# Kernel tuning notes

Measured on AMD Instinct MI355X. Metric: run time of the kernel, lower is better.

The kernel has to match this reference:

```python
import jax, jax.numpy as jnp
import numpy as np

N = 50000
E = 800000
F_IN = 128
HID = 64
HEADS = 4
NUM_TYPES = 1
NEG_SLOPE = 0.2


def setup_inputs() -> dict:
    key = jax.random.key(0)
    ks = jax.random.split(key, 20)
    s = 0.05
    inp = {
        "node_features": jax.random.normal(ks[0], (N, F_IN), jnp.float32),
        "node_types": jax.random.randint(ks[1], (N,), 0, NUM_TYPES, jnp.int32),
        "edge_index": jax.random.randint(ks[2], (2, E), 0, N, jnp.int32),
        # params
        "type_emb": jax.random.normal(ks[3], (NUM_TYPES, HID), jnp.float32) * s,
        "proj_w": jax.random.normal(ks[4], (F_IN, HID), jnp.float32) * s,
        "proj_b": jnp.zeros((HID,), jnp.float32),
        # GAT layer 0: in=64 -> heads*64, concat=True
        "lin_w0": jax.random.normal(ks[5], (HID, HEADS * HID), jnp.float32) * s,
        "att_src0": jax.random.normal(ks[6], (HEADS, HID), jnp.float32) * s,
        "att_dst0": jax.random.normal(ks[7], (HEADS, HID), jnp.float32) * s,
        "bias0": jnp.zeros((HEADS * HID,), jnp.float32),
        "ln_g0": jnp.ones((HEADS * HID,), jnp.float32),
        "ln_b0": jnp.zeros((HEADS * HID,), jnp.float32),
        # GAT layer 1: in=256 -> heads*64, concat=False (mean over heads)
        "lin_w1": jax.random.normal(ks[8], (HEADS * HID, HEADS * HID), jnp.float32) * s,
        "att_src1": jax.random.normal(ks[9], (HEADS, HID), jnp.float32) * s,
        "att_dst1": jax.random.normal(ks[10], (HEADS, HID), jnp.float32) * s,
        "bias1": jnp.zeros((HID,), jnp.float32),
        "ln_g1": jnp.ones((HID,), jnp.float32),
        "ln_b1": jnp.zeros((HID,), jnp.float32),
    }
    return inp


def _layer_norm(x, g, b, eps=1e-5):
    mu = jnp.mean(x, axis=-1, keepdims=True)
    var = jnp.mean(jnp.square(x - mu), axis=-1, keepdims=True)
    return (x - mu) * jax.lax.rsqrt(var + eps) * g + b


def _gat_conv(x, src, dst, lin_w, att_src, att_dst, bias, concat):
    # PyG GATConv: linear -> per-edge additive attention -> segment softmax over
    # incoming edges -> weighted scatter-sum. Self-loops already in src/dst.
    n = x.shape[0]
    H, C = att_src.shape
    h = (x @ lin_w).reshape(n, H, C)            # [N,H,C]
    a_s = jnp.sum(h * att_src[None], axis=-1)   # [N,H]
    a_d = jnp.sum(h * att_dst[None], axis=-1)   # [N,H]
    a = jax.nn.leaky_relu(a_s[src] + a_d[dst], NEG_SLOPE)  # [E,H]
    m = jax.ops.segment_max(a, dst, num_segments=n)
    e = jnp.exp(a - m[dst])
    z = jax.ops.segment_sum(e, dst, num_segments=n)
    alpha = e / z[dst]                           # [E,H]
    msg = h[src] * alpha[..., None]              # [E,H,C]
    out = jax.ops.segment_sum(msg, dst, num_segments=n)  # [N,H,C]
    if concat:
        out = out.reshape(n, H * C)
    else:
        out = out.mean(axis=1)
    return out + bias


def reference(node_features, node_types, edge_index,
              type_emb, proj_w, proj_b,
              lin_w0, att_src0, att_dst0, bias0, ln_g0, ln_b0,
              lin_w1, att_src1, att_dst1, bias1, ln_g1, ln_b1):
    n = node_features.shape[0]
    # add self loops (PyG GATConv default add_self_loops=True)
    loop = jnp.arange(n, dtype=edge_index.dtype)
    src = jnp.concatenate([edge_index[0], loop])
    dst = jnp.concatenate([edge_index[1], loop])

    x = node_features @ proj_w + proj_b + type_emb[node_types]  # [N,64]

    # layer 0: no residual (i == 0)
    x = _gat_conv(x, src, dst, lin_w0, att_src0, att_dst0, bias0, concat=True)
    x = jax.nn.relu(_layer_norm(x, ln_g0, ln_b0))  # [N,256]; dropout = identity (eval)

    # layer 1: residual shape [N,256] != output [N,64] -> residual skipped
    x = _gat_conv(x, src, dst, lin_w1, att_src1, att_dst1, bias1, concat=False)
    x = jax.nn.relu(_layer_norm(x, ln_g1, ln_b1))  # [N,64]
    return x
```

## Files before the change

### kernel.cpp

```cpp
#include <hip/hip_runtime.h>


#define BLK 256

typedef __bf16 bf16x8 __attribute__((ext_vector_type(8)));
typedef __bf16 bf16x4 __attribute__((ext_vector_type(4)));
typedef float  f32x4  __attribute__((ext_vector_type(4)));


__global__ __launch_bounds__(BLK) void k_deg(
    const int* __restrict__ dst, int* __restrict__ deg, int E, int n) {
  const int etot = E + n;
  for (int e = blockIdx.x * BLK + threadIdx.x; e < etot; e += gridDim.x * BLK) {
    int d = (e < E) ? dst[e] : (e - E);
    atomicAdd(&deg[d], 1);
  }
}

__global__ __launch_bounds__(BLK) void k_scan_chunk(
    const int* __restrict__ in, int* __restrict__ out, int* __restrict__ csum, int n) {
  const int b = blockIdx.x, t = threadIdx.x, i = b * BLK + t;
  const int lane = t & 63, w = t >> 6;
  int v = (i < n) ? in[i] : 0;
  int inc = v;
#pragma unroll
  for (int o = 1; o < 64; o <<= 1) {
    int tmp = __shfl_up(inc, o);
    if (lane >= o) inc += tmp;
  }
  __shared__ int ws[4];
  if (lane == 63) ws[w] = inc;
  __syncthreads();
  int off = 0;
  for (int k = 0; k < w; ++k) off += ws[k];
  if (i < n) out[i] = off + inc - v;
  if (t == BLK - 1 && csum) csum[b] = off + inc;
}

__global__ __launch_bounds__(BLK) void k_scan_add(
    int* __restrict__ rowstart, const int* __restrict__ chunkoff,
    int* __restrict__ cursor, int n) {
  for (int i = blockIdx.x * BLK + threadIdx.x; i < n; i += gridDim.x * BLK) {
    int r = rowstart[i] + chunkoff[i >> 8];
    rowstart[i] = r;
    cursor[i] = r;
  }
}

__global__ __launch_bounds__(BLK) void k_fill(
    const int* __restrict__ src, const int* __restrict__ dst,
    int* __restrict__ cursor, int* __restrict__ sidx, int E, int n) {
  const int etot = E + n;
  for (int e = blockIdx.x * BLK + threadIdx.x; e < etot; e += gridDim.x * BLK) {
    int s, d;
    if (e < E) { s = src[e]; d = dst[e]; } else { s = e - E; d = s; }
    int slot = atomicAdd(&cursor[d], 1);
    sidx[slot] = s;
  }
}


__global__ __launch_bounds__(BLK) void k_pack_w(
    const float* __restrict__ w, __bf16* __restrict__ wp, int K, int NC) {
  const int tot = (K >> 3) * NC;
  int idx = blockIdx.x * BLK + threadIdx.x;
  if (idx >= tot) return;
  int g = idx / NC, c = idx - g * NC;
#pragma unroll
  for (int j = 0; j < 8; ++j)
    wp[(size_t)idx * 8 + j] = (__bf16)w[(g * 8 + j) * NC + c];
}


__global__ __launch_bounds__(BLK) void k_proj_mfma(
    const float* __restrict__ nf, const int* __restrict__ types,
    const __bf16* __restrict__ pwp, const float* __restrict__ pb,
    const float* __restrict__ emb, __bf16* __restrict__ x0, int n) {
  const int t = threadIdx.x, w = t >> 6, l = t & 63;
  const int l15 = l & 15, lg = l >> 4;
  const int mbase = blockIdx.x * 64 + w * 16;
  f32x4 acc[4] = {};
  const int ar = mbase + l15;
  const bool av = ar < n;
#pragma unroll
  for (int ks = 0; ks < 4; ++ks) {
    bf16x8 a = {};
    if (av) {
      const float* ap = nf + (size_t)ar * 128 + ks * 32 + lg * 8;
      float4 f0 = *(const float4*)(ap);
      float4 f1 = *(const float4*)(ap + 4);
      a[0] = (__bf16)f0.x; a[1] = (__bf16)f0.y; a[2] = (__bf16)f0.z; a[3] = (__bf16)f0.w;
      a[4] = (__bf16)f1.x; a[5] = (__bf16)f1.y; a[6] = (__bf16)f1.z; a[7] = (__bf16)f1.w;
    }
#pragma unroll
    for (int nt = 0; nt < 4; ++nt) {
      int c = nt * 16 + l15;
      int g = ks * 4 + lg;
      bf16x8 b = *(const bf16x8*)(pwp + ((size_t)g * 64 + c) * 8);
      acc[nt] = __builtin_amdgcn_mfma_f32_16x16x32_bf16(a, b, acc[nt], 0, 0, 0);
    }
  }
#pragma unroll
  for (int reg = 0; reg < 4; ++reg) {
    int row = mbase + lg * 4 + reg;
    if (row < n) {
      int ty = types[row];
#pragma unroll
      for (int nt = 0; nt < 4; ++nt) {
        int c = nt * 16 + l15;
        x0[(size_t)row * 64 + c] = (__bf16)(acc[nt][reg] + pb[c] + emb[ty * 64 + c]);
      }
    }
  }
}


template <int K>
__global__ __launch_bounds__(BLK) void k_lin_mfma(
    const __bf16* __restrict__ X, const __bf16* __restrict__ Wp,
    const float* __restrict__ att_s, const float* __restrict__ att_d,
    __bf16* __restrict__ H, float* __restrict__ as_, float* __restrict__ ad_, int n) {
  const int t = threadIdx.x, w = t >> 6, l = t & 63;
  const int l15 = l & 15, lg = l >> 4;
  const int m0 = blockIdx.x * 64;

  float asv[4], adv[4];
#pragma unroll
  for (int nt = 0; nt < 4; ++nt) {
    int c = w * 64 + nt * 16 + l15;
    asv[nt] = att_s[c];
    adv[nt] = att_d[c];
  }

  f32x4 acc[4][4] = {};
  int rr[4];
  bool vv[4];
#pragma unroll
  for (int mt = 0; mt < 4; ++mt) { rr[mt] = m0 + mt * 16 + l15; vv[mt] = rr[mt] < n; }
  const bf16x8 zf = {};

  for (int ks = 0; ks < K / 32; ++ks) {
    bf16x8 a[4];
#pragma unroll
    for (int mt = 0; mt < 4; ++mt)
      a[mt] = vv[mt] ? *(const bf16x8*)(X + (size_t)rr[mt] * K + ks * 32 + lg * 8) : zf;
    bf16x8 b[4];
#pragma unroll
    for (int nt = 0; nt < 4; ++nt) {
      int c = w * 64 + nt * 16 + l15;
      int g = ks * 4 + lg;
      b[nt] = *(const bf16x8*)(Wp + ((size_t)g * 256 + c) * 8);
    }
#pragma unroll
    for (int nt = 0; nt < 4; ++nt)
#pragma unroll
      for (int mt = 0; mt < 4; ++mt)
        acc[mt][nt] = __builtin_amdgcn_mfma_f32_16x16x32_bf16(a[mt], b[nt], acc[mt][nt], 0, 0, 0);
  }

#pragma unroll
  for (int mt = 0; mt < 4; ++mt) {
#pragma unroll
    for (int reg = 0; reg < 4; ++reg) {
      int row = m0 + mt * 16 + lg * 4 + reg;
      bool vr = row < n;
      float s = 0.f, d = 0.f;
      if (vr) {
#pragma unroll
        for (int nt = 0; nt < 4; ++nt) {
          float cv = acc[mt][nt][reg];
          H[(size_t)row * 256 + w * 64 + nt * 16 + l15] = (__bf16)cv;
          s = fmaf(cv, asv[nt], s);
          d = fmaf(cv, adv[nt], d);
        }
      }
#pragma unroll
      for (int o = 8; o; o >>= 1) { s += __shfl_xor(s, o); d += __shfl_xor(d, o); }
      if (l15 == 0 && vr) { as_[row * 4 + w] = s; ad_[row * 4 + w] = d; }
    }
  }
}


__global__ __launch_bounds__(BLK) void k_agg0(
    const int* __restrict__ rowstart, const int* __restrict__ deg,
    const int* __restrict__ sidx, const float* __restrict__ as_,
    const float* __restrict__ ad_, const __bf16* __restrict__ h0,
    const float* __restrict__ bias, const float* __restrict__ g,
    const float* __restrict__ b, __bf16* __restrict__ x1, int n) {
  const int lane = threadIdx.x & 63;
  const int wid = (blockIdx.x * BLK + threadIdx.x) >> 6;
  const int nw = (gridDim.x * BLK) >> 6;
  const int hsel = lane >> 4;
  const float4 bias4 = ((const float4*)bias)[lane];
  const float4 g4 = ((const float4*)g)[lane];
  const float4 b4 = ((const float4*)b)[lane];
  for (int d = wid; d < n; d += nw) {
    const int start = rowstart[d], cnt = deg[d];
    const int* sp = sidx + start;
    const float adv = ad_[d * 4 + hsel];
    float ax = 0.f, ay = 0.f, az = 0.f, aw = 0.f, z = 0.f;
    int j = 0;
    for (; j + 4 <= cnt; j += 4) {
      int4 s4 = *(const int4*)(sp + j);
      int s0 = __builtin_amdgcn_readfirstlane(s4.x);
      int s1 = __builtin_amdgcn_readfirstlane(s4.y);
      int s2 = __builtin_amdgcn_readfirstlane(s4.z);
      int s3 = __builtin_amdgcn_readfirstlane(s4.w);
      float q0 = as_[s0 * 4 + hsel], q1 = as_[s1 * 4 + hsel];
      float q2 = as_[s2 * 4 + hsel], q3 = as_[s3 * 4 + hsel];
      bf16x4 v0 = *(const bf16x4*)(h0 + (size_t)s0 * 256 + lane * 4);
      bf16x4 v1 = *(const bf16x4*)(h0 + (size_t)s1 * 256 + lane * 4);
      bf16x4 v2 = *(const bf16x4*)(h0 + (size_t)s2 * 256 + lane * 4);
      bf16x4 v3 = *(const bf16x4*)(h0 + (size_t)s3 * 256 + lane * 4);
      float a;
      a = q0 + adv; a = fmaxf(a, 0.2f * a); float e0 = __expf(a);
      a = q1 + adv; a = fmaxf(a, 0.2f * a); float e1 = __expf(a);
      a = q2 + adv; a = fmaxf(a, 0.2f * a); float e2 = __expf(a);
      a = q3 + adv; a = fmaxf(a, 0.2f * a); float e3 = __expf(a);
      z += (e0 + e1) + (e2 + e3);
      ax = fmaf(e0, (float)v0[0], ax); ay = fmaf(e0, (float)v0[1], ay);
      az = fmaf(e0, (float)v0[2], az); aw = fmaf(e0, (float)v0[3], aw);
      ax = fmaf(e1, (float)v1[0], ax); ay = fmaf(e1, (float)v1[1], ay);
      az = fmaf(e1, (float)v1[2], az); aw = fmaf(e1, (float)v1[3], aw);
      ax = fmaf(e2, (float)v2[0], ax); ay = fmaf(e2, (float)v2[1], ay);
      az = fmaf(e2, (float)v2[2], az); aw = fmaf(e2, (float)v2[3], aw);
      ax = fmaf(e3, (float)v3[0], ax); ay = fmaf(e3, (float)v3[1], ay);
      az = fmaf(e3, (float)v3[2], az); aw = fmaf(e3, (float)v3[3], aw);
    }
    for (; j < cnt; ++j) {
      int s = __builtin_amdgcn_readfirstlane(sp[j]);
      float a = as_[s * 4 + hsel] + adv; a = fmaxf(a, 0.2f * a);
      float e = __expf(a);
      z += e;
      bf16x4 hv = *(const bf16x4*)(h0 + (size_t)s * 256 + lane * 4);
      ax = fmaf(e, (float)hv[0], ax); ay = fmaf(e, (float)hv[1], ay);
      az = fmaf(e, (float)hv[2], az); aw = fmaf(e, (float)hv[3], aw);
    }
    float rz = 1.f / z;
    float vx = ax * rz + bias4.x, vy = ay * rz + bias4.y;
    float vz = az * rz + bias4.z, vw = aw * rz + bias4.w;
    float s1 = vx + vy + vz + vw;
#pragma unroll
    for (int o = 32; o; o >>= 1) s1 += __shfl_xor(s1, o);
    float mu = s1 * (1.f / 256.f);
    float dx = vx - mu, dy = vy - mu, dz = vz - mu, dw = vw - mu;
    float q = dx * dx + dy * dy + dz * dz + dw * dw;
#pragma unroll
    for (int o = 32; o; o >>= 1) q += __shfl_xor(q, o);
    float is = rsqrtf(q * (1.f / 256.f) + 1e-5f);
    bf16x4 o4;
    o4[0] = (__bf16)fmaxf(dx * is * g4.x + b4.x, 0.f);
    o4[1] = (__bf16)fmaxf(dy * is * g4.y + b4.y, 0.f);
    o4[2] = (__bf16)fmaxf(dz * is * g4.z + b4.z, 0.f);
    o4[3] = (__bf16)fmaxf(dw * is * g4.w + b4.w, 0.f);
    *(bf16x4*)(x1 + (size_t)d * 256 + lane * 4) = o4;
  }
}

__global__ __launch_bounds__(BLK) void k_agg1(
    const int* __restrict__ rowstart, const int* __restrict__ deg,
    const int* __restrict__ sidx, const float* __restrict__ as_,
    const float* __restrict__ ad_, const __bf16* __restrict__ h1,
    const float* __restrict__ bias, const float* __restrict__ g,
    const float* __restrict__ b, float* __restrict__ out, int n) {
  const int lane = threadIdx.x & 63;
  const int wid = (blockIdx.x * BLK + threadIdx.x) >> 6;
  const int nw = (gridDim.x * BLK) >> 6;
  const int hsel = lane >> 4;
  const int p = lane & 15;
  const float4 bias4 = ((const float4*)bias)[p];
  const float4 g4 = ((const float4*)g)[p];
  const float4 b4 = ((const float4*)b)[p];
  for (int d = wid; d < n; d += nw) {
    const int start = rowstart[d], cnt = deg[d];
    const int* sp = sidx + start;
    const float adv = ad_[d * 4 + hsel];
    float ax = 0.f, ay = 0.f, az = 0.f, aw = 0.f, z = 0.f;
    int j = 0;
    for (; j + 4 <= cnt; j += 4) {
      int4 s4 = *(const int4*)(sp + j);
      int s0 = __builtin_amdgcn_readfirstlane(s4.x);
      int s1 = __builtin_amdgcn_readfirstlane(s4.y);
      int s2 = __builtin_amdgcn_readfirstlane(s4.z);
      int s3 = __builtin_amdgcn_readfirstlane(s4.w);
      float q0 = as_[s0 * 4 + hsel], q1 = as_[s1 * 4 + hsel];
      float q2 = as_[s2 * 4 + hsel], q3 = as_[s3 * 4 + hsel];
      bf16x4 v0 = *(const bf16x4*)(h1 + (size_t)s0 * 256 + lane * 4);
      bf16x4 v1 = *(const bf16x4*)(h1 + (size_t)s1 * 256 + lane * 4);
      bf16x4 v2 = *(const bf16x4*)(h1 + (size_t)s2 * 256 + lane * 4);
      bf16x4 v3 = *(const bf16x4*)(h1 + (size_t)s3 * 256 + lane * 4);
      float a;
      a = q0 + adv; a = fmaxf(a, 0.2f * a); float e0 = __expf(a);
      a = q1 + adv; a = fmaxf(a, 0.2f * a); float e1 = __expf(a);
      a = q2 + adv; a = fmaxf(a, 0.2f * a); float e2 = __expf(a);
      a = q3 + adv; a = fmaxf(a, 0.2f * a); float e3 = __expf(a);
      z += (e0 + e1) + (e2 + e3);
      ax = fmaf(e0, (float)v0[0], ax); ay = fmaf(e0, (float)v0[1], ay);
      az = fmaf(e0, (float)v0[2], az); aw = fmaf(e0, (float)v0[3], aw);
      ax = fmaf(e1, (float)v1[0], ax); ay = fmaf(e1, (float)v1[1], ay);
      az = fmaf(e1, (float)v1[2], az); aw = fmaf(e1, (float)v1[3], aw);
      ax = fmaf(e2, (float)v2[0], ax); ay = fmaf(e2, (float)v2[1], ay);
      az = fmaf(e2, (float)v2[2], az); aw = fmaf(e2, (float)v2[3], aw);
      ax = fmaf(e3, (float)v3[0], ax); ay = fmaf(e3, (float)v3[1], ay);
      az = fmaf(e3, (float)v3[2], az); aw = fmaf(e3, (float)v3[3], aw);
    }
    for (; j < cnt; ++j) {
      int s = __builtin_amdgcn_readfirstlane(sp[j]);
      float a = as_[s * 4 + hsel] + adv; a = fmaxf(a, 0.2f * a);
      float e = __expf(a);
      z += e;
      bf16x4 hv = *(const bf16x4*)(h1 + (size_t)s * 256 + lane * 4);
      ax = fmaf(e, (float)hv[0], ax); ay = fmaf(e, (float)hv[1], ay);
      az = fmaf(e, (float)hv[2], az); aw = fmaf(e, (float)hv[3], aw);
    }
    float rz = 1.f / z;
    ax *= rz; ay *= rz; az *= rz; aw *= rz;
#pragma unroll
    for (int o = 16; o <= 32; o <<= 1) {
      ax += __shfl_xor(ax, o); ay += __shfl_xor(ay, o);
      az += __shfl_xor(az, o); aw += __shfl_xor(aw, o);
    }
    float vx = 0.25f * ax + bias4.x, vy = 0.25f * ay + bias4.y;
    float vz = 0.25f * az + bias4.z, vw = 0.25f * aw + bias4.w;
    float s1 = vx + vy + vz + vw;
#pragma unroll
    for (int o = 8; o; o >>= 1) s1 += __shfl_xor(s1, o);
    float mu = s1 * (1.f / 64.f);
    float dx = vx - mu, dy = vy - mu, dz = vz - mu, dw = vw - mu;
    float q = dx * dx + dy * dy + dz * dz + dw * dw;
#pragma unroll
    for (int o = 8; o; o >>= 1) q += __shfl_xor(q, o);
    float is = rsqrtf(q * (1.f / 64.f) + 1e-5f);
    if (lane < 16) {
      float4 o4;
      o4.x = fmaxf(dx * is * g4.x + b4.x, 0.f);
      o4.y = fmaxf(dy * is * g4.y + b4.y, 0.f);
      o4.z = fmaxf(dz * is * g4.z + b4.z, 0.f);
      o4.w = fmaxf(dw * is * g4.w + b4.w, 0.f);
      ((float4*)(out + (size_t)d * 64))[p] = o4;
    }
  }
}

extern "C" void kernel_launch(void* const* d_in, const int* in_sizes, int n_in,
                              void* d_out, int out_size, void* d_ws, size_t ws_size,
                              hipStream_t stream) {
  const float* nf    = (const float*)d_in[0];
  const int*   types = (const int*)d_in[1];
  const int*   ei    = (const int*)d_in[2];
  const float* emb   = (const float*)d_in[3];
  const float* pw    = (const float*)d_in[4];
  const float* pb    = (const float*)d_in[5];
  const float* w0    = (const float*)d_in[6];
  const float* asrc0 = (const float*)d_in[7];
  const float* adst0 = (const float*)d_in[8];
  const float* b0    = (const float*)d_in[9];
  const float* g0    = (const float*)d_in[10];
  const float* be0   = (const float*)d_in[11];
  const float* w1    = (const float*)d_in[12];
  const float* asrc1 = (const float*)d_in[13];
  const float* adst1 = (const float*)d_in[14];
  const float* b1    = (const float*)d_in[15];
  const float* g1    = (const float*)d_in[16];
  const float* be1   = (const float*)d_in[17];

  const int n = in_sizes[0] / 128;
  const int E = in_sizes[2] / 2;
  const int etot = E + n;
  const int* srcI = ei;
  const int* dstI = ei + E;

  float* W = (float*)d_ws;
  size_t o = 0;
  __bf16* x0 = (__bf16*)(W + o); o += (size_t)n * 32;
  __bf16* h  = (__bf16*)(W + o); o += (size_t)n * 128;
  __bf16* x1 = (__bf16*)(W + o); o += (size_t)n * 128;
  float* as_ = W + o;            o += (size_t)n * 4;
  float* ad_ = W + o;            o += (size_t)n * 4;
  __bf16* w0p = (__bf16*)(W + o); o += 64 * 256 / 2;
  __bf16* w1p = (__bf16*)(W + o); o += 256 * 256 / 2;
  __bf16* pwp = (__bf16*)(W + o); o += 128 * 64 / 2;
  int* I = (int*)(W + o);
  size_t io = 0;
  int* deg      = I + io; io += n;
  int* rowstart = I + io; io += n;
  int* cursor   = I + io; io += n;
  int* csum     = I + io; io += 256;
  int* chunkoff = I + io; io += 256;
  int* sidx     = I + io; io += etot;

  const int nchunks = (n + BLK - 1) / BLK;
  const int mgrid = (n + 63) / 64;
  const int agrid = (n * 64 + BLK - 1) / BLK;

  hipMemsetAsync(deg, 0, (size_t)n * sizeof(int), stream);
  k_deg<<<1024, BLK, 0, stream>>>(dstI, deg, E, n);
  k_scan_chunk<<<nchunks, BLK, 0, stream>>>(deg, rowstart, csum, n);
  k_scan_chunk<<<1, BLK, 0, stream>>>(csum, chunkoff, nullptr, nchunks);
  k_scan_add<<<nchunks, BLK, 0, stream>>>(rowstart, chunkoff, cursor, n);
  k_fill<<<1024, BLK, 0, stream>>>(srcI, dstI, cursor, sidx, E, n);

  k_pack_w<<<8, BLK, 0, stream>>>(w0, w0p, 64, 256);
  k_pack_w<<<32, BLK, 0, stream>>>(w1, w1p, 256, 256);
  k_pack_w<<<4, BLK, 0, stream>>>(pw, pwp, 128, 64);

  k_proj_mfma<<<mgrid, BLK, 0, stream>>>(nf, types, pwp, pb, emb, x0, n);
  k_lin_mfma<64><<<mgrid, BLK, 0, stream>>>(x0, w0p, asrc0, adst0, h, as_, ad_, n);
  k_agg0<<<agrid, BLK, 0, stream>>>(rowstart, deg, sidx, as_, ad_, h, b0, g0, be0, x1, n);

  k_lin_mfma<256><<<mgrid, BLK, 0, stream>>>(x1, w1p, asrc1, adst1, h, as_, ad_, n);
  k_agg1<<<agrid, BLK, 0, stream>>>(rowstart, deg, sidx, as_, ad_, h, b1, g1, be1,
                                    (float*)d_out, n);
}
```

Before: 302.8 us.

## Merge independent launches into combined kernels and store attention logits in bf16

```diff
diff --git a/kernel.cpp b/kernel.cpp
--- a/kernel.cpp
+++ b/kernel.cpp
@@ -8,62 +8,10 @@
 typedef float  f32x4  __attribute__((ext_vector_type(4)));
 
 
-__global__ __launch_bounds__(BLK) void k_deg(
-    const int* __restrict__ dst, int* __restrict__ deg, int E, int n) {
-  const int etot = E + n;
-  for (int e = blockIdx.x * BLK + threadIdx.x; e < etot; e += gridDim.x * BLK) {
-    int d = (e < E) ? dst[e] : (e - E);
-    atomicAdd(&deg[d], 1);
-  }
-}
-
-__global__ __launch_bounds__(BLK) void k_scan_chunk(
-    const int* __restrict__ in, int* __restrict__ out, int* __restrict__ csum, int n) {
-  const int b = blockIdx.x, t = threadIdx.x, i = b * BLK + t;
-  const int lane = t & 63, w = t >> 6;
-  int v = (i < n) ? in[i] : 0;
-  int inc = v;
-#pragma unroll
-  for (int o = 1; o < 64; o <<= 1) {
-    int tmp = __shfl_up(inc, o);
-    if (lane >= o) inc += tmp;
-  }
-  __shared__ int ws[4];
-  if (lane == 63) ws[w] = inc;
-  __syncthreads();
-  int off = 0;
-  for (int k = 0; k < w; ++k) off += ws[k];
-  if (i < n) out[i] = off + inc - v;
-  if (t == BLK - 1 && csum) csum[b] = off + inc;
-}
-
-__global__ __launch_bounds__(BLK) void k_scan_add(
-    int* __restrict__ rowstart, const int* __restrict__ chunkoff,
-    int* __restrict__ cursor, int n) {
-  for (int i = blockIdx.x * BLK + threadIdx.x; i < n; i += gridDim.x * BLK) {
-    int r = rowstart[i] + chunkoff[i >> 8];
-    rowstart[i] = r;
-    cursor[i] = r;
-  }
-}
-
-__global__ __launch_bounds__(BLK) void k_fill(
-    const int* __restrict__ src, const int* __restrict__ dst,
-    int* __restrict__ cursor, int* __restrict__ sidx, int E, int n) {
-  const int etot = E + n;
-  for (int e = blockIdx.x * BLK + threadIdx.x; e < etot; e += gridDim.x * BLK) {
-    int s, d;
-    if (e < E) { s = src[e]; d = dst[e]; } else { s = e - E; d = s; }
-    int slot = atomicAdd(&cursor[d], 1);
-    sidx[slot] = s;
-  }
-}
-
-
-__global__ __launch_bounds__(BLK) void k_pack_w(
-    const float* __restrict__ w, __bf16* __restrict__ wp, int K, int NC) {
+__device__ __forceinline__ void pack_body(const float* __restrict__ w,
+                                          __bf16* __restrict__ wp,
+                                          int K, int NC, int idx) {
   const int tot = (K >> 3) * NC;
-  int idx = blockIdx.x * BLK + threadIdx.x;
   if (idx >= tot) return;
   int g = idx / NC, c = idx - g * NC;
 #pragma unroll
@@ -71,14 +19,13 @@
     wp[(size_t)idx * 8 + j] = (__bf16)w[(g * 8 + j) * NC + c];
 }
 
-
-__global__ __launch_bounds__(BLK) void k_proj_mfma(
-    const float* __restrict__ nf, const int* __restrict__ types,
+__device__ __forceinline__ void proj_body(
+    int bid, const float* __restrict__ nf, const int* __restrict__ types,
     const __bf16* __restrict__ pwp, const float* __restrict__ pb,
     const float* __restrict__ emb, __bf16* __restrict__ x0, int n) {
   const int t = threadIdx.x, w = t >> 6, l = t & 63;
   const int l15 = l & 15, lg = l >> 4;
-  const int mbase = blockIdx.x * 64 + w * 16;
+  const int mbase = bid * 64 + w * 16;
   f32x4 acc[4] = {};
   const int ar = mbase + l15;
   const bool av = ar < n;
@@ -114,15 +61,14 @@
   }
 }
 
-
 template <int K>
-__global__ __launch_bounds__(BLK) void k_lin_mfma(
-    const __bf16* __restrict__ X, const __bf16* __restrict__ Wp,
+__device__ __forceinline__ void lin_body(
+    int bid, const __bf16* __restrict__ X, const __bf16* __restrict__ Wp,
     const float* __restrict__ att_s, const float* __restrict__ att_d,
-    __bf16* __restrict__ H, float* __restrict__ as_, float* __restrict__ ad_, int n) {
+    __bf16* __restrict__ H, __bf16* __restrict__ asb, __bf16* __restrict__ adb, int n) {
   const int t = threadIdx.x, w = t >> 6, l = t & 63;
   const int l15 = l & 15, lg = l >> 4;
-  const int m0 = blockIdx.x * 64;
+  const int m0 = bid * 64;
 
   float asv[4], adv[4];
 #pragma unroll
@@ -176,16 +122,115 @@
       }
 #pragma unroll
       for (int o = 8; o; o >>= 1) { s += __shfl_xor(s, o); d += __shfl_xor(d, o); }
-      if (l15 == 0 && vr) { as_[row * 4 + w] = s; ad_[row * 4 + w] = d; }
-    }
-  }
+      if (l15 == 0 && vr) { asb[row * 4 + w] = (__bf16)s; adb[row * 4 + w] = (__bf16)d; }
+    }
+  }
+}
+
+
+__global__ __launch_bounds__(BLK) void k_prep(
+    const float* __restrict__ pw, const float* __restrict__ w0,
+    const float* __restrict__ w1, __bf16* __restrict__ pwp,
+    __bf16* __restrict__ w0p, __bf16* __restrict__ w1p,
+    int* __restrict__ deg, int n, int nchunks) {
+  int b = blockIdx.x;
+  const int t = threadIdx.x;
+  if (b < nchunks) { int i = b * BLK + t; if (i < n) deg[i] = 0; return; }
+  b -= nchunks;
+  if (b < 4)  { pack_body(pw, pwp, 128, 64,  b * BLK + t); return; }
+  b -= 4;
+  if (b < 8)  { pack_body(w0, w0p, 64, 256,  b * BLK + t); return; }
+  b -= 8;
+  pack_body(w1, w1p, 256, 256, b * BLK + t);
+}
+
+__global__ __launch_bounds__(BLK) void k_deg_proj(
+    const int* __restrict__ dst, int* __restrict__ deg, int E,
+    const float* __restrict__ nf, const int* __restrict__ types,
+    const __bf16* __restrict__ pwp, const float* __restrict__ pb,
+    const float* __restrict__ emb, __bf16* __restrict__ x0, int n) {
+  if (blockIdx.x < 1024) {
+    const int etot = E + n;
+    for (int e = blockIdx.x * BLK + threadIdx.x; e < etot; e += 1024 * BLK) {
+      int d = (e < E) ? dst[e] : (e - E);
+      atomicAdd(&deg[d], 1);
+    }
+    return;
+  }
+  proj_body(blockIdx.x - 1024, nf, types, pwp, pb, emb, x0, n);
+}
+
+__global__ __launch_bounds__(BLK) void k_scan_chunk(
+    const int* __restrict__ in, int* __restrict__ out, int* __restrict__ csum, int n) {
+  const int b = blockIdx.x, t = threadIdx.x, i = b * BLK + t;
+  const int lane = t & 63, w = t >> 6;
+  int v = (i < n) ? in[i] : 0;
+  int inc = v;
+#pragma unroll
+  for (int o = 1; o < 64; o <<= 1) {
+    int tmp = __shfl_up(inc, o);
+    if (lane >= o) inc += tmp;
+  }
+  __shared__ int ws[4];
+  if (lane == 63) ws[w] = inc;
+  __syncthreads();
+  int off = 0;
+  for (int k = 0; k < w; ++k) off += ws[k];
+  if (i < n) out[i] = off + inc - v;
+  if (t == BLK - 1) csum[b] = off + inc;
+}
+
+__global__ __launch_bounds__(BLK) void k_scan_add2(
+    int* __restrict__ rowstart, const int* __restrict__ csum,
+    int* __restrict__ cursor, int n, int nchunks) {
+  const int b = blockIdx.x, t = threadIdx.x;
+  const int lane = t & 63, w = t >> 6;
+  int v = (t < b && t < nchunks) ? csum[t] : 0;
+#pragma unroll
+  for (int o = 32; o; o >>= 1) v += __shfl_down(v, o);
+  __shared__ int ws[4];
+  if (lane == 0) ws[w] = v;
+  __syncthreads();
+  const int soff = ws[0] + ws[1] + ws[2] + ws[3];
+  int i = b * BLK + t;
+  if (i < n) {
+    int r = rowstart[i] + soff;
+    rowstart[i] = r;
+    cursor[i] = r;
+  }
+}
+
+__global__ __launch_bounds__(BLK) void k_fill_lin0(
+    const int* __restrict__ src, const int* __restrict__ dst,
+    int* __restrict__ cursor, int* __restrict__ sidx, int E,
+    const __bf16* __restrict__ x0, const __bf16* __restrict__ w0p,
+    const float* __restrict__ asrc0, const float* __restrict__ adst0,
+    __bf16* __restrict__ h, __bf16* __restrict__ asb, __bf16* __restrict__ adb, int n) {
+  if (blockIdx.x < 1024) {
+    const int etot = E + n;
+    for (int e = blockIdx.x * BLK + threadIdx.x; e < etot; e += 1024 * BLK) {
+      int s, d;
+      if (e < E) { s = src[e]; d = dst[e]; } else { s = e - E; d = s; }
+      int slot = atomicAdd(&cursor[d], 1);
+      sidx[slot] = s;
+    }
+    return;
+  }
+  lin_body<64>(blockIdx.x - 1024, x0, w0p, asrc0, adst0, h, asb, adb, n);
+}
+
+__global__ __launch_bounds__(BLK) void k_lin256(
+    const __bf16* __restrict__ X, const __bf16* __restrict__ Wp,
+    const float* __restrict__ att_s, const float* __restrict__ att_d,
+    __bf16* __restrict__ H, __bf16* __restrict__ asb, __bf16* __restrict__ adb, int n) {
+  lin_body<256>(blockIdx.x, X, Wp, att_s, att_d, H, asb, adb, n);
 }
 
 
 __global__ __launch_bounds__(BLK) void k_agg0(
     const int* __restrict__ rowstart, const int* __restrict__ deg,
-    const int* __restrict__ sidx, const float* __restrict__ as_,
-    const float* __restrict__ ad_, const __bf16* __restrict__ h0,
+    const int* __restrict__ sidx, const __bf16* __restrict__ asb,
+    const __bf16* __restrict__ adb, const __bf16* __restrict__ h0,
     const float* __restrict__ bias, const float* __restrict__ g,
     const float* __restrict__ b, __bf16* __restrict__ x1, int n) {
   const int lane = threadIdx.x & 63;
@@ -198,7 +243,7 @@
   for (int d = wid; d < n; d += nw) {
     const int start = rowstart[d], cnt = deg[d];
     const int* sp = sidx + start;
-    const float adv = ad_[d * 4 + hsel];
+    const float adv = (float)adb[d * 4 + hsel];
     float ax = 0.f, ay = 0.f, az = 0.f, aw = 0.f, z = 0.f;
     int j = 0;
     for (; j + 4 <= cnt; j += 4) {
@@ -207,8 +252,8 @@
       int s1 = __builtin_amdgcn_readfirstlane(s4.y);
       int s2 = __builtin_amdgcn_readfirstlane(s4.z);
       int s3 = __builtin_amdgcn_readfirstlane(s4.w);
-      float q0 = as_[s0 * 4 + hsel], q1 = as_[s1 * 4 + hsel];
-      float q2 = as_[s2 * 4 + hsel], q3 = as_[s3 * 4 + hsel];
+      float q0 = (float)asb[s0 * 4 + hsel], q1 = (float)asb[s1 * 4 + hsel];
+      float q2 = (float)asb[s2 * 4 + hsel], q3 = (float)asb[s3 * 4 + hsel];
       bf16x4 v0 = *(const bf16x4*)(h0 + (size_t)s0 * 256 + lane * 4);
       bf16x4 v1 = *(const bf16x4*)(h0 + (size_t)s1 * 256 + lane * 4);
       bf16x4 v2 = *(const bf16x4*)(h0 + (size_t)s2 * 256 + lane * 4);
@@ -230,7 +275,7 @@
     }
     for (; j < cnt; ++j) {
       int s = __builtin_amdgcn_readfirstlane(sp[j]);
-      float a = as_[s * 4 + hsel] + adv; a = fmaxf(a, 0.2f * a);
+      float a = (float)asb[s * 4 + hsel] + adv; a = fmaxf(a, 0.2f * a);
       float e = __expf(a);
       z += e;
       bf16x4 hv = *(const bf16x4*)(h0 + (size_t)s * 256 + lane * 4);
@@ -260,8 +305,8 @@
 
 __global__ __launch_bounds__(BLK) void k_agg1(
     const int* __restrict__ rowstart, const int* __restrict__ deg,
-    const int* __restrict__ sidx, const float* __restrict__ as_,
-    const float* __restrict__ ad_, const __bf16* __restrict__ h1,
+    const int* __restrict__ sidx, const __bf16* __restrict__ asb,
+    const __bf16* __restrict__ adb, const __bf16* __restrict__ h1,
     const float* __restrict__ bias, const float* __restrict__ g,
     const float* __restrict__ b, float* __restrict__ out, int n) {
   const int lane = threadIdx.x & 63;
@@ -275,7 +320,7 @@
   for (int d = wid; d < n; d += nw) {
     const int start = rowstart[d], cnt = deg[d];
     const int* sp = sidx + start;
-    const float adv = ad_[d * 4 + hsel];
+    const float adv = (float)adb[d * 4 + hsel];
     float ax = 0.f, ay = 0.f, az = 0.f, aw = 0.f, z = 0.f;
     int j = 0;
     for (; j + 4 <= cnt; j += 4) {
@@ -284,8 +329,8 @@
       int s1 = __builtin_amdgcn_readfirstlane(s4.y);
       int s2 = __builtin_amdgcn_readfirstlane(s4.z);
       int s3 = __builtin_amdgcn_readfirstlane(s4.w);
-      float q0 = as_[s0 * 4 + hsel], q1 = as_[s1 * 4 + hsel];
-      float q2 = as_[s2 * 4 + hsel], q3 = as_[s3 * 4 + hsel];
+      float q0 = (float)asb[s0 * 4 + hsel], q1 = (float)asb[s1 * 4 + hsel];
+      float q2 = (float)asb[s2 * 4 + hsel], q3 = (float)asb[s3 * 4 + hsel];
       bf16x4 v0 = *(const bf16x4*)(h1 + (size_t)s0 * 256 + lane * 4);
       bf16x4 v1 = *(const bf16x4*)(h1 + (size_t)s1 * 256 + lane * 4);
       bf16x4 v2 = *(const bf16x4*)(h1 + (size_t)s2 * 256 + lane * 4);
@@ -307,7 +352,7 @@
     }
     for (; j < cnt; ++j) {
       int s = __builtin_amdgcn_readfirstlane(sp[j]);
-      float a = as_[s * 4 + hsel] + adv; a = fmaxf(a, 0.2f * a);
+      float a = (float)asb[s * 4 + hsel] + adv; a = fmaxf(a, 0.2f * a);
       float e = __expf(a);
       z += e;
       bf16x4 hv = *(const bf16x4*)(h1 + (size_t)s * 256 + lane * 4);
@@ -373,11 +418,11 @@
 
   float* W = (float*)d_ws;
   size_t o = 0;
-  __bf16* x0 = (__bf16*)(W + o); o += (size_t)n * 32;
-  __bf16* h  = (__bf16*)(W + o); o += (size_t)n * 128;
-  __bf16* x1 = (__bf16*)(W + o); o += (size_t)n * 128;
-  float* as_ = W + o;            o += (size_t)n * 4;
-  float* ad_ = W + o;            o += (size_t)n * 4;
+  __bf16* x0  = (__bf16*)(W + o); o += (size_t)n * 32;
+  __bf16* h   = (__bf16*)(W + o); o += (size_t)n * 128;
+  __bf16* x1  = (__bf16*)(W + o); o += (size_t)n * 128;
+  __bf16* asb = (__bf16*)(W + o); o += (size_t)n * 2;
+  __bf16* adb = (__bf16*)(W + o); o += (size_t)n * 2;
   __bf16* w0p = (__bf16*)(W + o); o += 64 * 256 / 2;
   __bf16* w1p = (__bf16*)(W + o); o += 256 * 256 / 2;
   __bf16* pwp = (__bf16*)(W + o); o += 128 * 64 / 2;
@@ -387,29 +432,20 @@
   int* rowstart = I + io; io += n;
   int* cursor   = I + io; io += n;
   int* csum     = I + io; io += 256;
-  int* chunkoff = I + io; io += 256;
   int* sidx     = I + io; io += etot;
 
   const int nchunks = (n + BLK - 1) / BLK;
   const int mgrid = (n + 63) / 64;
   const int agrid = (n * 64 + BLK - 1) / BLK;
 
-  hipMemsetAsync(deg, 0, (size_t)n * sizeof(int), stream);
-  k_deg<<<1024, BLK, 0, stream>>>(dstI, deg, E, n);
+  k_prep<<<nchunks + 44, BLK, 0, stream>>>(pw, w0, w1, pwp, w0p, w1p, deg, n, nchunks);
+  k_deg_proj<<<1024 + mgrid, BLK, 0, stream>>>(dstI, deg, E, nf, types, pwp, pb, emb, x0, n);
   k_scan_chunk<<<nchunks, BLK, 0, stream>>>(deg, rowstart, csum, n);
-  k_scan_chunk<<<1, BLK, 0, stream>>>(csum, chunkoff, nullptr, nchunks);
-  k_scan_add<<<nchunks, BLK, 0, stream>>>(rowstart, chunkoff, cursor, n);
-  k_fill<<<1024, BLK, 0, stream>>>(srcI, dstI, cursor, sidx, E, n);
-
-  k_pack_w<<<8, BLK, 0, stream>>>(w0, w0p, 64, 256);
-  k_pack_w<<<32, BLK, 0, stream>>>(w1, w1p, 256, 256);
-  k_pack_w<<<4, BLK, 0, stream>>>(pw, pwp, 128, 64);
-
-  k_proj_mfma<<<mgrid, BLK, 0, stream>>>(nf, types, pwp, pb, emb, x0, n);
-  k_lin_mfma<64><<<mgrid, BLK, 0, stream>>>(x0, w0p, asrc0, adst0, h, as_, ad_, n);
-  k_agg0<<<agrid, BLK, 0, stream>>>(rowstart, deg, sidx, as_, ad_, h, b0, g0, be0, x1, n);
-
-  k_lin_mfma<256><<<mgrid, BLK, 0, stream>>>(x1, w1p, asrc1, adst1, h, as_, ad_, n);
-  k_agg1<<<agrid, BLK, 0, stream>>>(rowstart, deg, sidx, as_, ad_, h, b1, g1, be1,
+  k_scan_add2<<<nchunks, BLK, 0, stream>>>(rowstart, csum, cursor, n, nchunks);
+  k_fill_lin0<<<1024 + mgrid, BLK, 0, stream>>>(srcI, dstI, cursor, sidx, E,
+                                                x0, w0p, asrc0, adst0, h, asb, adb, n);
+  k_agg0<<<agrid, BLK, 0, stream>>>(rowstart, deg, sidx, asb, adb, h, b0, g0, be0, x1, n);
+  k_lin256<<<mgrid, BLK, 0, stream>>>(x1, w1p, asrc1, adst1, h, asb, adb, n);
+  k_agg1<<<agrid, BLK, 0, stream>>>(rowstart, deg, sidx, asb, adb, h, b1, g1, be1,
                                     (float*)d_out, n);
 }
```

Measured after the change: 287.7 us. -5.0%, faster.
